# Performance work log

Hardware: AMD Instinct MI355X
Metric: run time of the kernel (lower is better)

Reference implementation:

```python
import jax, jax.numpy as jnp
import numpy as np
from jax import lax

FORGET_BIAS = 1.0
EPS = 1e-12


def l2_normalize_time(x):
    # tf.nn.l2_normalize(x, dim=1): normalize over the timestep axis
    sq = jnp.sum(jnp.square(x), axis=1, keepdims=True)
    return x * lax.rsqrt(jnp.maximum(sq, EPS))


def lstm_layer(x, W, b, units):
    """TF LSTMCell: kernel (in+units, 4*units), gates split as i, j, f, o.
    x: [B, T, D] -> [B, T, units]"""
    B = x.shape[0]

    def step(carry, xt):
        c, h = carry
        z = jnp.concatenate([xt, h], axis=-1) @ W + b  # [B, 4*units]
        i, j, f, o = jnp.split(z, 4, axis=-1)
        c = jax.nn.sigmoid(f + FORGET_BIAS) * c + jax.nn.sigmoid(i) * jnp.tanh(j)
        h = jax.nn.sigmoid(o) * jnp.tanh(c)
        return (c, h), h

    init = (jnp.zeros((B, units), x.dtype), jnp.zeros((B, units), x.dtype))
    _, hs = lax.scan(step, init, jnp.swapaxes(x, 0, 1))  # [T, B, units]
    return jnp.swapaxes(hs, 0, 1)


def setup_inputs() -> dict:
    key = jax.random.key(0)
    ks = jax.random.split(key, 5)
    B, T, U = 256, 2048, 64
    x = jax.random.normal(ks[0], (B, T, 1), dtype=jnp.float32)
    # layer 0: LSTMCell(64), input dim 1 -> kernel (1+64, 4*64)
    W0 = jax.random.normal(ks[1], (1 + U, 4 * U), dtype=jnp.float32) * 0.05
    b0 = jnp.zeros((4 * U,), dtype=jnp.float32)
    # layer 1: LSTMCell(1), input dim 64 -> kernel (64+1, 4)
    W1 = jax.random.normal(ks[2], (U + 1, 4), dtype=jnp.float32) * 0.05
    b1 = jnp.zeros((4,), dtype=jnp.float32)
    # dense(1)
    Wd = jax.random.normal(ks[3], (1, 1), dtype=jnp.float32)
    bd = jnp.zeros((1,), dtype=jnp.float32)
    return {"x": x, "W0": W0, "b0": b0, "W1": W1, "b1": b1, "Wd": Wd, "bd": bd}


def reference(x, W0, b0, W1, b1, Wd, bd):
    h = l2_normalize_time(x)          # [B, T, 1]
    h = lstm_layer(h, W0, b0, 64)     # [B, T, 64]
    h = lstm_layer(h, W1, b1, 1)      # [B, T, 1]
    out = h @ Wd + bd                 # dense(1), no activation
    return out
```

## Files before the change

### kernel.cpp

```cpp
#include <hip/hip_runtime.h>
#include <math.h>

#define TT 2048
#define UU 64
#define BB 256
#define NTHR 192

typedef float v2f __attribute__((ext_vector_type(2)));
typedef float v4f __attribute__((ext_vector_type(4)));

__device__ __forceinline__ float frcp(float x) { return __builtin_amdgcn_rcpf(x); }
__device__ __forceinline__ float fsigmoid(float x) { return frcp(1.0f + __expf(-x)); }
__device__ __forceinline__ float ftanh(float x) { return 1.0f - 2.0f * frcp(1.0f + __expf(2.0f * x)); }

__device__ __forceinline__ void pkfma_ll(v2f& a, v2f h, v2f w) {
    asm("v_pk_fma_f32 %0, %1, %2, %0 op_sel:[0,0,0] op_sel_hi:[0,1,1]"
        : "+v"(a) : "v"(h), "v"(w));
}
__device__ __forceinline__ void pkfma_hh(v2f& a, v2f h, v2f w) {
    asm("v_pk_fma_f32 %0, %1, %2, %0 op_sel:[1,0,0] op_sel_hi:[1,1,1]"
        : "+v"(a) : "v"(h), "v"(w));
}

__global__
__attribute__((amdgpu_flat_work_group_size(NTHR, NTHR)))
__attribute__((amdgpu_waves_per_eu(1, 1)))
void lstm_ts_kernel(
    const float* __restrict__ x, const float* __restrict__ W0,
    const float* __restrict__ b0, const float* __restrict__ W1,
    const float* __restrict__ b1, const float* __restrict__ Wd,
    const float* __restrict__ bd, float* __restrict__ out)
{
    __shared__ __align__(16) float xbuf[TT];
    __shared__ __align__(16) float ringP[2][2][UU];
    __shared__ __align__(16) v4f  zpart[2][2][UU];
    __shared__ float red[3];

    const int tid = threadIdx.x;
    const int wid = tid >> 6;
    const int u = tid & 63;
    const int b = blockIdx.x;
    const float* xrow = x + b * TT;
    float* outrow = out + b * TT;

    float ss = 0.f;
    for (int i = tid; i < TT; i += NTHR) {
        float v = xrow[i];
        xbuf[i] = v;
        ss += v * v;
    }
    #pragma unroll
    for (int m = 1; m < 64; m <<= 1) ss += __shfl_xor(ss, m, 64);
    if (u == 0) red[wid] = ss;
    if (wid < 2) ringP[wid][1][u] = 0.f;
    __syncthreads();

    if (wid < 2) {
        const int koff = 32 * wid;
        const float sq = (red[0] + red[1]) + red[2];
        const float scale = 1.0f / sqrtf(fmaxf(sq, 1e-12f));

        #define DECLW(k) v2f WI##k, WF##k; { \
            const float* r_ = W0 + (1 + koff + (k)) * 256; \
            WI##k.x = r_[u];       WI##k.y = r_[64 + u]; \
            WF##k.x = r_[128 + u]; WF##k.y = r_[192 + u]; } \
            asm volatile("" : "+v"(WI##k)); asm volatile("" : "+v"(WF##k));
        DECLW(0)  DECLW(1)  DECLW(2)  DECLW(3)  DECLW(4)  DECLW(5)  DECLW(6)  DECLW(7)
        DECLW(8)  DECLW(9)  DECLW(10) DECLW(11) DECLW(12) DECLW(13) DECLW(14) DECLW(15)
        DECLW(16) DECLW(17) DECLW(18) DECLW(19) DECLW(20) DECLW(21) DECLW(22) DECLW(23)
        DECLW(24) DECLW(25) DECLW(26) DECLW(27) DECLW(28) DECLW(29) DECLW(30) DECLW(31)
        #undef DECLW

        const float sel = (wid == 0) ? 1.f : 0.f;
        const float wxi = W0[u] * scale * sel,       wxj = W0[64 + u] * scale * sel;
        const float wxf = W0[128 + u] * scale * sel, wxo = W0[192 + u] * scale * sel;
        const float bci = b0[u] * sel,       bcj = b0[64 + u] * sel;
        const float bcf = b0[128 + u] * sel, bco = b0[192 + u] * sel;

        float c0 = 0.f;

        for (int t = 0; t < TT; ++t) {
            const float xr = xbuf[t];
            const float* hs = &ringP[wid][(t + 1) & 1][koff];

            v2f ai0, ai1 = 0.f, af0, af1 = 0.f;
            ai0.x = fmaf(xr, wxi, bci); ai0.y = fmaf(xr, wxj, bcj);
            af0.x = fmaf(xr, wxf, bcf); af0.y = fmaf(xr, wxo, bco);

            #define MACR(m, A, B, C, D, E, F, G, H) { \
                v4f hv_ = *(const v4f*)(hs + 4 * (m)); \
                v2f h01_ = __builtin_shufflevector(hv_, hv_, 0, 1); \
                v2f h23_ = __builtin_shufflevector(hv_, hv_, 2, 3); \
                pkfma_ll(ai0, h01_, A); pkfma_ll(af0, h01_, E); \
                pkfma_hh(ai1, h01_, B); pkfma_hh(af1, h01_, F); \
                pkfma_ll(ai0, h23_, C); pkfma_ll(af0, h23_, G); \
                pkfma_hh(ai1, h23_, D); pkfma_hh(af1, h23_, H); \
            }
            MACR(0, WI0,  WI1,  WI2,  WI3,  WF0,  WF1,  WF2,  WF3)
            MACR(1, WI4,  WI5,  WI6,  WI7,  WF4,  WF5,  WF6,  WF7)
            MACR(2, WI8,  WI9,  WI10, WI11, WF8,  WF9,  WF10, WF11)
            MACR(3, WI12, WI13, WI14, WI15, WF12, WF13, WF14, WF15)
            MACR(4, WI16, WI17, WI18, WI19, WF16, WF17, WF18, WF19)
            MACR(5, WI20, WI21, WI22, WI23, WF20, WF21, WF22, WF23)
            MACR(6, WI24, WI25, WI26, WI27, WF24, WF25, WF26, WF27)
            MACR(7, WI28, WI29, WI30, WI31, WF28, WF29, WF30, WF31)
            #undef MACR

            const v2f pij = ai0 + ai1;
            const v2f pfo = af0 + af1;
            v4f zp; zp.x = pij.x; zp.y = pij.y; zp.z = pfo.x; zp.w = pfo.y;
            zpart[t & 1][wid][u] = zp;
            __syncthreads();

            const v4f zo4 = zpart[t & 1][1 - wid][u];
            const float zi = pij.x + zo4.x;
            const float zj = pij.y + zo4.y;
            const float zf = pfo.x + zo4.z;
            const float zo = pfo.y + zo4.w;

            c0 = fsigmoid(zf + 1.0f) * c0 + fsigmoid(zi) * ftanh(zj);
            const float h = fsigmoid(zo) * ftanh(c0);

            ringP[wid][t & 1][u] = h;
        }
        __syncthreads();
    } else {
        const float w1v0 = W1[u * 4 + 0], w1v1 = W1[u * 4 + 1];
        const float w1v2 = W1[u * 4 + 2], w1v3 = W1[u * 4 + 3];
        const float w1h0 = W1[256], w1h1 = W1[257], w1h2 = W1[258], w1h3 = W1[259];
        const float b10 = b1[0], b11 = b1[1], b12 = b1[2], b13 = b1[3];
        const float wd = Wd[0], bdv = bd[0];

        float c1 = 0.f, h1 = 0.f, oval = 0.f;

        #define L1STEP(s) { \
            const float hu = ringP[0][(s) & 1][u];   \
            float p0 = hu * w1v0, p1 = hu * w1v1, p2 = hu * w1v2, p3 = hu * w1v3; \
            _Pragma("unroll") \
            for (int m = 1; m < 64; m <<= 1) { \
                p0 += __shfl_xor(p0, m, 64); \
                p1 += __shfl_xor(p1, m, 64); \
                p2 += __shfl_xor(p2, m, 64); \
                p3 += __shfl_xor(p3, m, 64); \
            } \
            const float z1i = p0 + fmaf(h1, w1h0, b10); \
            const float z1j = p1 + fmaf(h1, w1h1, b11); \
            const float z1f = p2 + fmaf(h1, w1h2, b12); \
            const float z1o = p3 + fmaf(h1, w1h3, b13); \
            c1 = fsigmoid(z1f + 1.0f) * c1 + fsigmoid(z1i) * ftanh(z1j); \
            h1 = fsigmoid(z1o) * ftanh(c1); \
            const float ov = fmaf(h1, wd, bdv); \
            if (((s) & 63) == u) oval = ov; \
            if (((s) & 63) == 63) outrow[((s) & ~63) + u] = oval; \
        }

        for (int t = 0; t < TT; ++t) {
            __syncthreads();
            if (t > 0) L1STEP(t - 1)
        }
        __syncthreads();
        L1STEP(TT - 1)
        #undef L1STEP
    }
}

extern "C" void kernel_launch(void* const* d_in, const int* in_sizes, int n_in,
                              void* d_out, int out_size, void* d_ws, size_t ws_size,
                              hipStream_t stream) {
    const float* x  = (const float*)d_in[0];
    const float* W0 = (const float*)d_in[1];
    const float* b0 = (const float*)d_in[2];
    const float* W1 = (const float*)d_in[3];
    const float* b1 = (const float*)d_in[4];
    const float* Wd = (const float*)d_in[5];
    const float* bd = (const float*)d_in[6];
    float* out = (float*)d_out;
    lstm_ts_kernel<<<BB, NTHR, 0, stream>>>(x, W0, b0, W1, b1, Wd, bd, out);
}
```

Before: 959.4 us.

## Replace per-step block barrier with LDS flag handshake and chunked layer-1 consumption

```diff
diff --git a/kernel.cpp b/kernel.cpp
--- a/kernel.cpp
+++ b/kernel.cpp
@@ -5,6 +5,9 @@
 #define UU 64
 #define BB 256
 #define NTHR 192
+#define CH 16
+#define NCH (TT / CH)
+#define NSLOT 32
 
 typedef float v2f __attribute__((ext_vector_type(2)));
 typedef float v4f __attribute__((ext_vector_type(4)));
@@ -32,8 +35,9 @@
     const float* __restrict__ bd, float* __restrict__ out)
 {
     __shared__ __align__(16) float xbuf[TT];
-    __shared__ __align__(16) float ringP[2][2][UU];
+    __shared__ __align__(16) float ringP[2][NSLOT][UU];
     __shared__ __align__(16) v4f  zpart[2][2][UU];
+    __shared__ int flagL[2];
     __shared__ float red[3];
 
     const int tid = threadIdx.x;
@@ -52,7 +56,8 @@
     #pragma unroll
     for (int m = 1; m < 64; m <<= 1) ss += __shfl_xor(ss, m, 64);
     if (u == 0) red[wid] = ss;
-    if (wid < 2) ringP[wid][1][u] = 0.f;
+    if (wid < 2) ringP[wid][NSLOT - 1][u] = 0.f;
+    if (tid < 2) flagL[tid] = 0;
     __syncthreads();
 
     if (wid < 2) {
@@ -81,7 +86,7 @@
 
         for (int t = 0; t < TT; ++t) {
             const float xr = xbuf[t];
-            const float* hs = &ringP[wid][(t + 1) & 1][koff];
+            const float* hs = &ringP[wid][(t + NSLOT - 1) & (NSLOT - 1)][koff];
 
             v2f ai0, ai1 = 0.f, af0, af1 = 0.f;
             ai0.x = fmaf(xr, wxi, bci); ai0.y = fmaf(xr, wxj, bcj);
@@ -110,7 +115,10 @@
             const v2f pfo = af0 + af1;
             v4f zp; zp.x = pij.x; zp.y = pij.y; zp.z = pfo.x; zp.w = pfo.y;
             zpart[t & 1][wid][u] = zp;
-            __syncthreads();
+
+            asm volatile("s_waitcnt lgkmcnt(0)" ::: "memory");
+            if (u == 0) flagL[wid] = t + 1;
+            while (*(volatile int*)&flagL[1 - wid] < t + 1) {}
 
             const v4f zo4 = zpart[t & 1][1 - wid][u];
             const float zi = pij.x + zo4.x;
@@ -121,9 +129,10 @@
             c0 = fsigmoid(zf + 1.0f) * c0 + fsigmoid(zi) * ftanh(zj);
             const float h = fsigmoid(zo) * ftanh(c0);
 
-            ringP[wid][t & 1][u] = h;
+            ringP[wid][t & (NSLOT - 1)][u] = h;
+
+            if ((t & (CH - 1)) == (CH - 1)) __syncthreads();
         }
-        __syncthreads();
     } else {
         const float w1v0 = W1[u * 4 + 0], w1v1 = W1[u * 4 + 1];
         const float w1v2 = W1[u * 4 + 2], w1v3 = W1[u * 4 + 3];
@@ -133,34 +142,31 @@
 
         float c1 = 0.f, h1 = 0.f, oval = 0.f;
 
-        #define L1STEP(s) { \
-            const float hu = ringP[0][(s) & 1][u];   \
-            float p0 = hu * w1v0, p1 = hu * w1v1, p2 = hu * w1v2, p3 = hu * w1v3; \
-            _Pragma("unroll") \
-            for (int m = 1; m < 64; m <<= 1) { \
-                p0 += __shfl_xor(p0, m, 64); \
-                p1 += __shfl_xor(p1, m, 64); \
-                p2 += __shfl_xor(p2, m, 64); \
-                p3 += __shfl_xor(p3, m, 64); \
-            } \
-            const float z1i = p0 + fmaf(h1, w1h0, b10); \
-            const float z1j = p1 + fmaf(h1, w1h1, b11); \
-            const float z1f = p2 + fmaf(h1, w1h2, b12); \
-            const float z1o = p3 + fmaf(h1, w1h3, b13); \
-            c1 = fsigmoid(z1f + 1.0f) * c1 + fsigmoid(z1i) * ftanh(z1j); \
-            h1 = fsigmoid(z1o) * ftanh(c1); \
-            const float ov = fmaf(h1, wd, bdv); \
-            if (((s) & 63) == u) oval = ov; \
-            if (((s) & 63) == 63) outrow[((s) & ~63) + u] = oval; \
+        for (int k2 = 0; k2 < NCH; ++k2) {
+            __syncthreads();
+            const int sbase = k2 * CH;
+            for (int si = 0; si < CH; ++si) {
+                const int s = sbase + si;
+                const float hu = ringP[0][s & (NSLOT - 1)][u];
+                float p0 = hu * w1v0, p1 = hu * w1v1, p2 = hu * w1v2, p3 = hu * w1v3;
+                #pragma unroll
+                for (int m = 1; m < 64; m <<= 1) {
+                    p0 += __shfl_xor(p0, m, 64);
+                    p1 += __shfl_xor(p1, m, 64);
+                    p2 += __shfl_xor(p2, m, 64);
+                    p3 += __shfl_xor(p3, m, 64);
+                }
+                const float z1i = p0 + fmaf(h1, w1h0, b10);
+                const float z1j = p1 + fmaf(h1, w1h1, b11);
+                const float z1f = p2 + fmaf(h1, w1h2, b12);
+                const float z1o = p3 + fmaf(h1, w1h3, b13);
+                c1 = fsigmoid(z1f + 1.0f) * c1 + fsigmoid(z1i) * ftanh(z1j);
+                h1 = fsigmoid(z1o) * ftanh(c1);
+                const float ov = fmaf(h1, wd, bdv);
+                if ((s & 63) == u) oval = ov;
+                if ((s & 63) == 63) outrow[(s & ~63) + u] = oval;
+            }
         }
-
-        for (int t = 0; t < TT; ++t) {
-            __syncthreads();
-            if (t > 0) L1STEP(t - 1)
-        }
-        __syncthreads();
-        L1STEP(TT - 1)
-        #undef L1STEP
     }
 }
 
```

New measurement: 1.083 ms. 12.9% more time.
